# Kernel tuning notes

Hardware: AMD Instinct MI355X
Metric: run time of the kernel (lower is better)

Reference implementation:

```python
import jax, jax.numpy as jnp
import numpy as np

B, L, D, N, NBLK = 16, 2048, 256, 64, 6  # 6 S4D layers: blocks 1,2,3,5 + 2 inner layers of FS4Ddeq


def setup_inputs() -> dict:
    key = jax.random.key(0)
    ks = jax.random.split(key, 12)
    x = jax.random.normal(ks[0], (B, L), dtype=jnp.float32)
    W_emb = jax.random.normal(ks[1], (1, D), dtype=jnp.float32) * 0.1
    b_emb = jnp.zeros((D,), jnp.float32)
    # S4D parameters, stacked over the 6 layers
    log_dt = jax.random.uniform(ks[2], (NBLK, D), minval=float(np.log(1e-3)), maxval=float(np.log(1e-1)), dtype=jnp.float32)
    logAre = jnp.full((NBLK, D, N), float(np.log(0.5)), jnp.float32)
    Aim = jnp.broadcast_to(jnp.pi * jnp.arange(N, dtype=jnp.float32), (NBLK, D, N)) * jnp.ones((NBLK, D, N), jnp.float32)
    Cre = jax.random.normal(ks[3], (NBLK, D, N), dtype=jnp.float32) * (0.5 ** 0.5)
    Cim = jax.random.normal(ks[4], (NBLK, D, N), dtype=jnp.float32) * (0.5 ** 0.5)
    Dskip = jax.random.normal(ks[5], (NBLK, D), dtype=jnp.float32)
    Wout = jax.random.normal(ks[6], (NBLK, D, D), dtype=jnp.float32) / np.sqrt(D)
    bout = jnp.zeros((NBLK, D), jnp.float32)
    gamma = jnp.ones((NBLK, D), jnp.float32)
    beta = jnp.zeros((NBLK, D), jnp.float32)
    # feedforward of the FS4Ddeq block (feed_size=[B,L,emb_dim], feed_act='relu')
    feed_W1 = jax.random.normal(ks[7], (D, D), dtype=jnp.float32) / np.sqrt(D)
    feed_b1 = jnp.zeros((D,), jnp.float32)
    feed_W2 = jax.random.normal(ks[8], (D, D), dtype=jnp.float32) / np.sqrt(D)
    feed_b2 = jnp.zeros((D,), jnp.float32)
    fc_W = jax.random.normal(ks[9], (D, 2), dtype=jnp.float32) / np.sqrt(D)
    fc_b = jnp.zeros((2,), jnp.float32)
    return dict(x=x, W_emb=W_emb, b_emb=b_emb, log_dt=log_dt, logAre=logAre, Aim=Aim,
                Cre=Cre, Cim=Cim, Dskip=Dskip, Wout=Wout, bout=bout, gamma=gamma, beta=beta,
                feed_W1=feed_W1, feed_b1=feed_b1, feed_W2=feed_W2, feed_b2=feed_b2,
                fc_W=fc_W, fc_b=fc_b)


def _s4d_block(h, log_dt, logAre, Aim, Cre, Cim, Dskip, Wout, bout, gamma, beta):
    """Pre-norm (BN eval-mode) -> diagonal SSM (ZOH, FFT conv) -> GELU -> Linear -> residual."""
    _, Lh, _ = h.shape
    z = gamma * h + beta  # BatchNorm in eval mode with identity running stats
    dt = jnp.exp(log_dt)[:, None]                      # [D,1]
    A = -jnp.exp(logAre) + 1j * Aim                    # [D,N] diagonal state matrix
    dtA = dt * A                                       # [D,N]
    C = (Cre + 1j * Cim) * (jnp.exp(dtA) - 1.0) / A    # ZOH-discretized C*B
    # Vandermonde kernel K[d,l] = 2*Re sum_n C[d,n] * exp(dtA[d,n])^l
    vand = jnp.exp(dtA[:, :, None] * jnp.arange(Lh, dtype=jnp.float32))  # [D,N,L]
    K = 2.0 * jnp.einsum('dn,dnl->dl', C, vand).real   # [D,L]
    u = jnp.transpose(z, (0, 2, 1))                    # [B,D,L]
    kf = jnp.fft.rfft(K, n=2 * Lh)
    uf = jnp.fft.rfft(u, n=2 * Lh)
    y = jnp.fft.irfft(uf * kf, n=2 * Lh)[..., :Lh]     # causal conv
    y = y + Dskip[:, None] * u                         # feedthrough D
    y = jax.nn.gelu(jnp.transpose(y, (0, 2, 1)))       # [B,L,D]
    y = jnp.einsum('bld,de->ble', y, Wout) + bout      # output projection
    return y + h                                       # skip connection


def reference(x, W_emb, b_emb, log_dt, logAre, Aim, Cre, Cim, Dskip, Wout, bout,
              gamma, beta, feed_W1, feed_b1, feed_W2, feed_b2, fc_W, fc_b):
    h = x[..., None] @ W_emb + b_emb  # nn.Linear(1, emb_dim): [B,L,D]
    # layers 1,2,3,5: S4D blocks (dropout is identity in eval mode)
    for i in range(4):
        h = _s4d_block(h, log_dt[i], logAre[i], Aim[i], Cre[i], Cim[i],
                       Dskip[i], Wout[i], bout[i], gamma[i], beta[i])
    # layer4: FS4Ddeq_model with layers=2 inner S4D blocks + relu feed net + final relu + skip
    r = h
    for i in (4, 5):
        h = _s4d_block(h, log_dt[i], logAre[i], Aim[i], Cre[i], Cim[i],
                       Dskip[i], Wout[i], bout[i], gamma[i], beta[i])
    h = jax.nn.relu(h @ feed_W1 + feed_b1) @ feed_W2 + feed_b2
    h = jax.nn.relu(h + r)
    mean_y = jnp.mean(h, axis=1)       # [B,D]
    logits = mean_y @ fc_W + fc_b      # [B,2]
    return logits
```

## Files before the change

kernel.cpp:

```cpp
#include <hip/hip_runtime.h>
#include <hip/hip_fp16.h>
#include <math.h>

#define B_ 16
#define L_ 2048
#define D_ 256
#define N_ 64
#define NBLK_ 6
#define LC_ 128
#define NC_ 16

typedef _Float16 half8 __attribute__((ext_vector_type(8)));
typedef float f32x4 __attribute__((ext_vector_type(4)));

__device__ __forceinline__ unsigned short f2h(float f) {
  _Float16 h = (_Float16)f;
  return *(unsigned short*)&h;
}
__device__ __forceinline__ float h2f(unsigned short u) {
  _Float16 h = *(_Float16*)&u;
  return (float)h;
}

__global__ void precompute_kernel(const float* __restrict__ log_dt,
                                  const float* __restrict__ logAre,
                                  const float* __restrict__ Aim,
                                  const float* __restrict__ Cre,
                                  const float* __restrict__ Cim,
                                  float* __restrict__ wbuf,
                                  float* __restrict__ c2buf,
                                  float* __restrict__ wlbuf) {
  int idx = blockIdx.x * blockDim.x + threadIdx.x;
  if (idx >= NBLK_ * D_ * N_) return;
  int blk = idx >> 14;
  int rem = idx & 16383;
  int d = rem >> 6;
  int n = rem & 63;
  float dt   = expf(log_dt[blk * D_ + d]);
  float are  = -expf(logAre[idx]);
  float aim  = Aim[idx];
  float dtar = dt * are, dtai = dt * aim;
  float er = expf(dtar);
  float wr = er * cosf(dtai);
  float wi = er * sinf(dtai);
  float inv = 1.0f / (are * are + aim * aim);
  float wm1r = wr - 1.0f;
  float br = (wm1r * are + wi * aim) * inv;
  float bi = (wi * are - wm1r * aim) * inv;
  float crv = Cre[idx], civ = Cim[idx];
  float c2r = 2.0f * (crv * br - civ * bi);
  float c2i = 2.0f * (crv * bi + civ * br);
  float eL = expf((float)LC_ * dtar);
  float angL = (float)LC_ * dtai;
  float* wb = wbuf + (size_t)((blk << 8) + d) * 128;
  wb[n] = wr; wb[64 + n] = wi;
  float* cb = c2buf + (size_t)((blk << 8) + d) * 128;
  cb[n] = c2r; cb[64 + n] = c2i;
  wlbuf[2 * idx] = eL * cosf(angL); wlbuf[2 * idx + 1] = eL * sinf(angL);
}

__global__ __launch_bounds__(256) void embed_trans(const float* __restrict__ x,
    const float* __restrict__ wemb, const float* __restrict__ bemb,
    unsigned short* __restrict__ H, unsigned short* __restrict__ UT) {
  __shared__ __align__(16) unsigned short lds[64][136];
  int bi = blockIdx.x;
  int bc = bi >> 2, dq = bi & 3;
  int b = bc >> 4, ch = bc & 15;
  int tid = threadIdx.x;
  int tau0 = tid >> 4;
  int dl = (tid & 15) << 2;
  float w4[4], b4[4];
#pragma unroll
  for (int i = 0; i < 4; ++i) {
    w4[i] = wemb[dq * 64 + dl + i];
    b4[i] = bemb[dq * 64 + dl + i];
  }
  for (int tt = 0; tt < 128; tt += 16) {
    int l = ch * 128 + tt + tau0;
    float xv = x[b * L_ + l];
    ushort4 hv;
    float v0 = fmaf(xv, w4[0], b4[0]);
    float v1 = fmaf(xv, w4[1], b4[1]);
    float v2 = fmaf(xv, w4[2], b4[2]);
    float v3 = fmaf(xv, w4[3], b4[3]);
    hv.x = f2h(v0); hv.y = f2h(v1); hv.z = f2h(v2); hv.w = f2h(v3);
    lds[dl + 0][tt + tau0] = hv.x;
    lds[dl + 1][tt + tau0] = hv.y;
    lds[dl + 2][tt + tau0] = hv.z;
    lds[dl + 3][tt + tau0] = hv.w;
    *(ushort4*)(H + ((size_t)(b * L_ + l)) * D_ + dq * 64 + dl) = hv;
  }
  __syncthreads();
  int r = tid >> 2, seg = (tid & 3) << 5;
  unsigned short* dst = UT + ((size_t)((dq * 64 + r) * 256 + bc)) * 128 + seg;
  const unsigned short* srow = &lds[r][seg];
  *(uint4*)(dst + 0)  = *(const uint4*)(srow + 0);
  *(uint4*)(dst + 8)  = *(const uint4*)(srow + 8);
  *(uint4*)(dst + 16) = *(const uint4*)(srow + 16);
  *(uint4*)(dst + 24) = *(const uint4*)(srow + 24);
}

__global__ __launch_bounds__(512) void scan_fused(
    const unsigned short* __restrict__ UT,
    const float* __restrict__ WB, const float* __restrict__ C2B,
    const float* __restrict__ WLB,
    const float* __restrict__ gamma_, const float* __restrict__ beta_,
    const float* __restrict__ dskip,
    unsigned short* __restrict__ GT, int blk) {
  __shared__ __align__(16) unsigned short SLl[256 * 136];
  __shared__ __align__(16) unsigned short Bm1[128 * 136];
  __shared__ __align__(16) unsigned short Bm2[128 * 136];
  __shared__ float wc[256];
  __shared__ float Kt[128];
  __shared__ float Pb[128];
  __shared__ float Sb[128];
  int d = blockIdx.x;
  int tid = threadIdx.x, lane = tid & 63, w = tid >> 6;
  int wm = (w & 3) << 6;
  int wn = (w >> 2) << 6;
  int cn = lane & 15, rq = lane >> 4;
  int ko = rq << 3;
  const unsigned short* Au = UT + (size_t)d * 256 * 128;

  half8 afr[4][4];
#pragma unroll
  for (int kc2 = 0; kc2 < 4; ++kc2)
#pragma unroll
    for (int mf = 0; mf < 4; ++mf)
      afr[kc2][mf] = *(const half8*)(Au + (size_t)(wm + (mf << 4) + cn) * 128 + (kc2 << 5) + ko);

  if (tid < 128) wc[tid] = WB[(size_t)((blk << 8) + d) * 128 + tid];
  else if (tid < 256) wc[tid] = C2B[(size_t)((blk << 8) + d) * 128 + (tid - 128)];
  __syncthreads();
  int n = tid & 63;
  float gd = gamma_[blk * D_ + d], bd = beta_[blk * D_ + d], dsk = dskip[blk * D_ + d];
  {
    float wr = wc[n], wi = wc[64 + n];
    float c2r = wc[128 + n], c2i = wc[192 + n];
    int j0 = w << 4;
    float pr = 1.f, pi = 0.f, br = wr, bi = wi;
    int e = j0;
    while (e) {
      if (e & 1) { float tt = pr * br - pi * bi; pi = pr * bi + pi * br; pr = tt; }
      float t2 = br * br - bi * bi; bi = 2.f * br * bi; br = t2;
      e >>= 1;
    }
    for (int k2 = 0; k2 < 16; ++k2) {
      int j = j0 + k2;
      Bm1[n * 136 + (127 - j)]        = f2h(gd * pr);
      Bm1[(64 + n) * 136 + (127 - j)] = f2h(-gd * pi);
      float qr = pr * wr - pi * wi, qi = pr * wi + pi * wr;
      Bm2[j * 136 + n]      = f2h(c2r * qr - c2i * qi);
      Bm2[j * 136 + 64 + n] = f2h(c2r * qi + c2i * qr);
      float kc = c2r * pr - c2i * pi;
#pragma unroll
      for (int off = 1; off < 64; off <<= 1) kc += __shfl_xor(kc, off);
      if (n == 0) Kt[j] = kc + (j == 0 ? dsk : 0.f);
      pr = qr; pi = qi;
    }
  }
  if (tid < 64) {
    const float* wlp = WLB + (((size_t)((blk << 8) + d)) * 64 + tid) * 2;
    float wlr = wlp[0], wli = wlp[1];
    float nr = wlr - 1.f, ni = wli;
    float dr2 = wc[tid] - 1.f, di = wc[64 + tid];
    float iv = 1.f / (dr2 * dr2 + di * di);
    Sb[tid]      = bd * ((nr * dr2 + ni * di) * iv);
    Sb[64 + tid] = bd * (-((ni * dr2 - nr * di) * iv));
  }
  __syncthreads();

  {
    f32x4 acc[4][4];
#pragma unroll
    for (int a = 0; a < 4; ++a)
#pragma unroll
      for (int b2 = 0; b2 < 4; ++b2) acc[a][b2] = (f32x4){0.f, 0.f, 0.f, 0.f};
#pragma unroll
    for (int kc = 0; kc < 4; ++kc) {
      half8 bf4[4];
#pragma unroll
      for (int nf = 0; nf < 4; ++nf)
        bf4[nf] = *(const half8*)((const _Float16*)Bm1 + (wn + (nf << 4) + cn) * 136 + (kc << 5) + ko);
#pragma unroll
      for (int mf = 0; mf < 4; ++mf)
#pragma unroll
        for (int nf = 0; nf < 4; ++nf)
          acc[mf][nf] = __builtin_amdgcn_mfma_f32_16x16x32_f16(afr[kc][mf], bf4[nf], acc[mf][nf], 0, 0, 0);
    }
#pragma unroll
    for (int nf = 0; nf < 4; ++nf) {
      int nl = wn + (nf << 4) + cn;
      float sb = Sb[nl];
#pragma unroll
      for (int mf = 0; mf < 4; ++mf)
#pragma unroll
        for (int rr = 0; rr < 4; ++rr) {
          int row = wm + (mf << 4) + (rq << 2) + rr;
          SLl[row * 136 + nl] = f2h(acc[mf][nf][rr] + sb);
        }
    }
  }
  __syncthreads();

  if (tid < 128) {
    float ps = 0.f;
    for (int t2 = 0; t2 <= tid; ++t2) ps += Kt[t2];
    Pb[tid] = bd * ps;
  }
  for (int task = tid; task < 1024; task += 512) {
    int b = task >> 6, nn = task & 63;
    const float* wlp = WLB + (((size_t)((blk << 8) + d)) * 64 + nn) * 2;
    float wlr = wlp[0], wli = wlp[1];
    float Sr = 0.f, Sj = 0.f;
    int row0 = b << 4;
    float tr2 = h2f(SLl[row0 * 136 + nn]);
    float tj2 = h2f(SLl[row0 * 136 + 64 + nn]);
    for (int c = 0; c < NC_; ++c) {
      int row = row0 + c;
      float ntr = 0.f, ntj = 0.f;
      if (c < NC_ - 1) {
        ntr = h2f(SLl[(row + 1) * 136 + nn]);
        ntj = h2f(SLl[(row + 1) * 136 + 64 + nn]);
      }
      SLl[row * 136 + nn]      = f2h(Sr);
      SLl[row * 136 + 64 + nn] = f2h(Sj);
      float nSr = fmaf(wlr, Sr, fmaf(wli, Sj, tr2));
      Sj = fmaf(-wli, Sr, fmaf(wlr, Sj, tj2));
      Sr = nSr;
      tr2 = ntr; tj2 = ntj;
    }
  }
  __syncthreads();

  {
    int chunk = tid & 15, rg = tid >> 4;
#pragma unroll
    for (int it = 0; it < 4; ++it) {
      int trow = (it << 5) + rg;
      int tau0 = chunk << 3;
      unsigned short v[8];
#pragma unroll
      for (int i = 0; i < 8; ++i) {
        int tau = tau0 + i;
        v[i] = (tau <= trow) ? f2h(gd * Kt[trow - tau]) : (unsigned short)0;
      }
      *(uint4*)(Bm1 + (size_t)trow * 136 + tau0) = *(uint4*)v;
    }
  }
  __syncthreads();

  {
    f32x4 acc[4][4];
#pragma unroll
    for (int a = 0; a < 4; ++a)
#pragma unroll
      for (int b2 = 0; b2 < 4; ++b2) acc[a][b2] = (f32x4){0.f, 0.f, 0.f, 0.f};
#pragma unroll
    for (int kb = 0; kb < 8; ++kb) {
      int kc = (kb & 3) << 5;
      half8 af[4], bf4[4];
      if (kb < 4) {
#pragma unroll
        for (int mf = 0; mf < 4; ++mf) af[mf] = afr[kb][mf];
#pragma unroll
        for (int nf = 0; nf < 4; ++nf)
          bf4[nf] = *(const half8*)((const _Float16*)Bm1 + (wn + (nf << 4) + cn) * 136 + kc + ko);
      } else {
#pragma unroll
        for (int mf = 0; mf < 4; ++mf)
          af[mf] = *(const half8*)((const _Float16*)SLl + (wm + (mf << 4) + cn) * 136 + kc + ko);
#pragma unroll
        for (int nf = 0; nf < 4; ++nf)
          bf4[nf] = *(const half8*)((const _Float16*)Bm2 + (wn + (nf << 4) + cn) * 136 + kc + ko);
      }
#pragma unroll
      for (int mf = 0; mf < 4; ++mf)
#pragma unroll
        for (int nf = 0; nf < 4; ++nf)
          acc[mf][nf] = __builtin_amdgcn_mfma_f32_16x16x32_f16(af[mf], bf4[nf], acc[mf][nf], 0, 0, 0);
    }
    __syncthreads();
    unsigned short* epi = SLl;
#pragma unroll
    for (int nf = 0; nf < 4; ++nf) {
      int nl = wn + (nf << 4) + cn;
      float pb2 = Pb[nl];
#pragma unroll
      for (int mf = 0; mf < 4; ++mf)
#pragma unroll
        for (int rr = 0; rr < 4; ++rr) {
          int ml = wm + (mf << 4) + (rq << 2) + rr;
          float xx = acc[mf][nf][rr] + pb2;
          float x3 = xx * xx * xx;
          float inner = 0.7978845608028654f * fmaf(0.044715f, x3, xx);
          float e = __expf(-2.f * fabsf(inner));
          float th = (1.f - e) / (1.f + e);
          th = copysignf(th, inner);
          epi[ml * 136 + nl] = f2h(0.5f * xx * (1.f + th));
        }
    }
    __syncthreads();
    int mr = tid >> 1, hf = (tid & 1) << 6;
    size_t gb = ((size_t)d * 256 + mr) * 128 + hf;
#pragma unroll
    for (int k = 0; k < 8; ++k)
      *(uint4*)(GT + gb + k * 8) = *(const uint4*)&epi[mr * 136 + hf + k * 8];
  }
}

__global__ void wprep_kernel(const float* __restrict__ Wout, const float* __restrict__ fW1,
                             const float* __restrict__ fW2, unsigned short* __restrict__ WT) {
  __shared__ float tile[64][65];
  int wv = blockIdx.x >> 4;
  int tk = (blockIdx.x >> 2) & 3;
  int tn = blockIdx.x & 3;
  const float* src = (wv < 6) ? (Wout + (size_t)wv * 65536) : (wv == 6 ? fW1 : fW2);
  int r = threadIdx.x >> 4;
  int c = (threadIdx.x & 15) << 2;
  for (int rr = 0; rr < 64; rr += 16) {
    float4 v = *(const float4*)(src + (size_t)(tk * 64 + r + rr) * 256 + tn * 64 + c);
    tile[r + rr][c] = v.x; tile[r + rr][c + 1] = v.y;
    tile[r + rr][c + 2] = v.z; tile[r + rr][c + 3] = v.w;
  }
  __syncthreads();
  for (int rr = 0; rr < 64; rr += 16) {
    int n = r + rr;
    ushort4 o;
    o.x = f2h(tile[c + 0][n]); o.y = f2h(tile[c + 1][n]);
    o.z = f2h(tile[c + 2][n]); o.w = f2h(tile[c + 3][n]);
    *(ushort4*)(WT + (size_t)wv * 65536 + (size_t)(tn * 64 + n) * 256 + tk * 64 + c) = o;
  }
}

__global__ __launch_bounds__(256, 2) void gemm_gt(const unsigned short* __restrict__ GT,
    const unsigned short* __restrict__ Wt, const float* __restrict__ bias,
    const unsigned short* __restrict__ res, unsigned short* __restrict__ hout,
    unsigned short* __restrict__ ut_next) {
  __shared__ __align__(16) unsigned short smem[18432];
  unsigned short* As = smem;
  unsigned short* Bs = smem + 9216;
  int tid = threadIdx.x;
  int bid = blockIdx.x;
  int bc = bid & 255;
  int m0 = bc * 128, n0 = (bid >> 8) << 7;
  int lane = tid & 63, w = tid >> 6;
  int wm = (w & 1) << 6, wn = (w >> 1) << 6;
  int rb = tid >> 3, cb = (tid & 7) << 3;
  int dr = tid >> 2, sg = (tid & 3) << 5;
  f32x4 acc[4][4];
#pragma unroll
  for (int mf = 0; mf < 4; ++mf)
#pragma unroll
    for (int nf = 0; nf < 4; ++nf) acc[mf][nf] = (f32x4){0.f, 0.f, 0.f, 0.f};

  uint4 gv[4], bv[4];
  {
    const uint4* grow = (const uint4*)(GT + ((size_t)(dr * 256 + bc)) * 128 + sg);
    gv[0] = grow[0]; gv[1] = grow[1]; gv[2] = grow[2]; gv[3] = grow[3];
#pragma unroll
    for (int rr = 0; rr < 4; ++rr)
      bv[rr] = *(const uint4*)(Wt + (size_t)(n0 + rb + rr * 32) * 256 + cb);
  }
  for (int kb = 0; kb < 4; ++kb) {
    __syncthreads();
    const unsigned short* pv = (const unsigned short*)gv;
#pragma unroll
    for (int i = 0; i < 32; ++i) As[(sg + i) * 72 + dr] = pv[i];
#pragma unroll
    for (int rr = 0; rr < 4; ++rr) *(uint4*)&Bs[(rb + rr * 32) * 72 + cb] = bv[rr];
    __syncthreads();
    if (kb < 3) {
      int k0 = (kb + 1) << 6;
      const uint4* grow = (const uint4*)(GT + ((size_t)((k0 + dr) * 256 + bc)) * 128 + sg);
      gv[0] = grow[0]; gv[1] = grow[1]; gv[2] = grow[2]; gv[3] = grow[3];
#pragma unroll
      for (int rr = 0; rr < 4; ++rr)
        bv[rr] = *(const uint4*)(Wt + (size_t)(n0 + rb + rr * 32) * 256 + k0 + cb);
    }
#pragma unroll
    for (int kw = 0; kw < 2; ++kw) {
      int ko = (kw << 5) + ((lane >> 4) << 3);
      half8 af[4], bfr[4];
#pragma unroll
      for (int mf = 0; mf < 4; ++mf)
        af[mf] = *(const half8*)&As[(wm + (mf << 4) + (lane & 15)) * 72 + ko];
#pragma unroll
      for (int nf = 0; nf < 4; ++nf)
        bfr[nf] = *(const half8*)&Bs[(wn + (nf << 4) + (lane & 15)) * 72 + ko];
#pragma unroll
      for (int mf = 0; mf < 4; ++mf)
#pragma unroll
        for (int nf = 0; nf < 4; ++nf)
          acc[mf][nf] = __builtin_amdgcn_mfma_f32_16x16x32_f16(af[mf], bfr[nf], acc[mf][nf], 0, 0, 0);
    }
  }
  int cn = lane & 15, rq = lane >> 4;
  __syncthreads();
  unsigned short* epi = smem;
#pragma unroll
  for (int nf = 0; nf < 4; ++nf) {
    int nl = wn + (nf << 4) + cn;
    float bv2 = bias[n0 + nl];
#pragma unroll
    for (int mf = 0; mf < 4; ++mf)
#pragma unroll
      for (int r = 0; r < 4; ++r) {
        int ml = wm + (mf << 4) + (rq << 2) + r;
        float v = acc[mf][nf][r] + bv2 + h2f(res[(size_t)(m0 + ml) * 256 + n0 + nl]);
        epi[ml * 136 + nl] = f2h(v);
      }
  }
  __syncthreads();
  {
    int mr = tid >> 1, hf = (tid & 1) << 6;
    unsigned short* dst = hout + (size_t)(m0 + mr) * 256 + n0 + hf;
    const unsigned short* srow = epi + mr * 136 + hf;
#pragma unroll
    for (int k = 0; k < 8; ++k) *(uint4*)(dst + k * 8) = *(const uint4*)(srow + k * 8);
  }
  if (ut_next) {
    int nl = tid >> 1, h2 = (tid & 1) << 6;
    unsigned short* dst = ut_next + ((size_t)(n0 + nl) * 256 + bc) * 128 + h2;
#pragma unroll
    for (int k = 0; k < 8; ++k) {
      unsigned short v8[8];
#pragma unroll
      for (int e = 0; e < 8; ++e) v8[e] = epi[(h2 + k * 8 + e) * 136 + nl];
      *(uint4*)(dst + k * 8) = *(uint4*)v8;
    }
  }
}

__global__ __launch_bounds__(256, 2) void gemm_ffn(const unsigned short* __restrict__ A,
    const unsigned short* __restrict__ Wt, const float* __restrict__ bias,
    const unsigned short* __restrict__ res, unsigned short* __restrict__ outp) {
  __shared__ __align__(16) unsigned short smem[18432];
  unsigned short* As = smem;
  unsigned short* Bs = smem + 9216;
  int tid = threadIdx.x;
  int bid = blockIdx.x;
  int m0 = (bid & 255) << 7, n0 = (bid >> 8) << 7;
  int lane = tid & 63, w = tid >> 6;
  int wm = (w & 1) << 6, wn = (w >> 1) << 6;
  int r0 = tid >> 3;
  int c0 = (tid & 7) << 3;
  f32x4 acc[4][4];
#pragma unroll
  for (int mf = 0; mf < 4; ++mf)
#pragma unroll
    for (int nf = 0; nf < 4; ++nf) acc[mf][nf] = (f32x4){0.f, 0.f, 0.f, 0.f};

  uint4 av[4], bv[4];
#pragma unroll
  for (int rr = 0; rr < 4; ++rr) {
    int r = r0 + rr * 32;
    av[rr] = *(const uint4*)(A + (size_t)(m0 + r) * 256 + c0);
    bv[rr] = *(const uint4*)(Wt + (size_t)(n0 + r) * 256 + c0);
  }
  for (int kb = 0; kb < 4; ++kb) {
    __syncthreads();
#pragma unroll
    for (int rr = 0; rr < 4; ++rr) {
      int r = r0 + rr * 32;
      *(uint4*)&As[r * 72 + c0] = av[rr];
      *(uint4*)&Bs[r * 72 + c0] = bv[rr];
    }
    __syncthreads();
    if (kb < 3) {
      int k0 = (kb + 1) << 6;
#pragma unroll
      for (int rr = 0; rr < 4; ++rr) {
        int r = r0 + rr * 32;
        av[rr] = *(const uint4*)(A + (size_t)(m0 + r) * 256 + k0 + c0);
        bv[rr] = *(const uint4*)(Wt + (size_t)(n0 + r) * 256 + k0 + c0);
      }
    }
#pragma unroll
    for (int kw = 0; kw < 2; ++kw) {
      int ko = (kw << 5) + ((lane >> 4) << 3);
      half8 af[4], bfr[4];
#pragma unroll
      for (int mf = 0; mf < 4; ++mf)
        af[mf] = *(const half8*)&As[(wm + (mf << 4) + (lane & 15)) * 72 + ko];
#pragma unroll
      for (int nf = 0; nf < 4; ++nf)
        bfr[nf] = *(const half8*)&Bs[(wn + (nf << 4) + (lane & 15)) * 72 + ko];
#pragma unroll
      for (int mf = 0; mf < 4; ++mf)
#pragma unroll
        for (int nf = 0; nf < 4; ++nf)
          acc[mf][nf] = __builtin_amdgcn_mfma_f32_16x16x32_f16(af[mf], bfr[nf], acc[mf][nf], 0, 0, 0);
    }
  }
  int cn = lane & 15, rq = lane >> 4;
  __syncthreads();
  unsigned short* epi = smem;
#pragma unroll
  for (int nf = 0; nf < 4; ++nf) {
    int nl = wn + (nf << 4) + cn;
#pragma unroll
    for (int r = 0; r < 4; ++r) {
#pragma unroll
      for (int mf = 0; mf < 4; ++mf) {
        int ml = wm + (mf << 4) + (rq << 2) + r;
        epi[ml * 136 + nl] = f2h(acc[mf][nf][r]);
      }
    }
  }
  __syncthreads();
  int mr = tid >> 1, hf = (tid & 1) << 6;
  unsigned short* dst = outp + (size_t)(m0 + mr) * 256 + n0 + hf;
#pragma unroll
  for (int k = 0; k < 8; ++k) {
    uint4 c = *(const uint4*)&epi[mr * 136 + hf + k * 8];
    uint4 rv = (uint4){0, 0, 0, 0};
    if (res) rv = *(const uint4*)(res + (size_t)(m0 + mr) * 256 + n0 + hf + k * 8);
    const unsigned short* cp = (const unsigned short*)&c;
    const unsigned short* rp = (const unsigned short*)&rv;
    unsigned short o8[8];
#pragma unroll
    for (int e = 0; e < 8; ++e) {
      float v = h2f(cp[e]) + bias[n0 + hf + k * 8 + e];
      if (res) v += h2f(rp[e]);
      o8[e] = f2h(fmaxf(v, 0.f));
    }
    *(uint4*)(dst + k * 8) = *(uint4*)o8;
  }
}

__global__ void head1_kernel(const unsigned short* __restrict__ H, float* __restrict__ part) {
  int b = blockIdx.x, ls = blockIdx.y, d = threadIdx.x;
  const unsigned short* p = H + ((size_t)(b * L_ + ls * 128)) * D_ + d;
  float sum = 0.f;
  for (int l = 0; l < 128; ++l) sum += h2f(p[(size_t)l * D_]);
  part[(b * 16 + ls) * D_ + d] = sum;
}

__global__ void head2_kernel(const float* __restrict__ part, const float* __restrict__ fcW,
                             const float* __restrict__ fcb, float* __restrict__ out) {
  int b = blockIdx.x, d = threadIdx.x;
  float sum = 0.f;
  for (int i = 0; i < 16; ++i) sum += part[(b * 16 + i) * D_ + d];
  __shared__ float meanv[D_];
  meanv[d] = sum * (1.0f / (float)L_);
  __syncthreads();
  if (d < 2) {
    float accv = fcb[d];
    for (int k = 0; k < D_; ++k) accv = fmaf(meanv[k], fcW[k * 2 + d], accv);
    out[b * 2 + d] = accv;
  }
}

extern "C" void kernel_launch(void* const* d_in, const int* in_sizes, int n_in,
                              void* d_out, int out_size, void* d_ws, size_t ws_size,
                              hipStream_t stream) {
  const float* x      = (const float*)d_in[0];
  const float* W_emb  = (const float*)d_in[1];
  const float* b_emb  = (const float*)d_in[2];
  const float* log_dt = (const float*)d_in[3];
  const float* logAre = (const float*)d_in[4];
  const float* Aim    = (const float*)d_in[5];
  const float* Cre    = (const float*)d_in[6];
  const float* Cim    = (const float*)d_in[7];
  const float* Dskip  = (const float*)d_in[8];
  const float* Wout   = (const float*)d_in[9];
  const float* bout   = (const float*)d_in[10];
  const float* gamma_ = (const float*)d_in[11];
  const float* beta_  = (const float*)d_in[12];
  const float* fW1    = (const float*)d_in[13];
  const float* fb1    = (const float*)d_in[14];
  const float* fW2    = (const float*)d_in[15];
  const float* fb2    = (const float*)d_in[16];
  const float* fcW    = (const float*)d_in[17];
  const float* fcb    = (const float*)d_in[18];
  float* outp = (float*)d_out;

  const size_t HSZ = (size_t)B_ * L_ * D_;
  float* WB     = (float*)d_ws;
  float* C2B    = WB + (size_t)NBLK_ * D_ * 128;
  float* WLB    = C2B + (size_t)NBLK_ * D_ * 128;
  unsigned short* H   = (unsigned short*)(WLB + (size_t)NBLK_ * D_ * N_ * 2);
  unsigned short* R   = H + HSZ;
  unsigned short* UT  = R + HSZ;
  unsigned short* GT  = UT + HSZ;
  unsigned short* Gbf = GT;
  unsigned short* WT  = GT + HSZ;

  precompute_kernel<<<(NBLK_ * D_ * N_ + 255) / 256, 256, 0, stream>>>(
      log_dt, logAre, Aim, Cre, Cim, WB, C2B, WLB);
  wprep_kernel<<<128, 256, 0, stream>>>(Wout, fW1, fW2, WT);
  embed_trans<<<1024, 256, 0, stream>>>(x, W_emb, b_emb, H, UT);

  const unsigned short* hin_t[6]  = {H, H, H, H, R, H};
  unsigned short*       hout_t[6] = {H, H, H, R, H, H};
  for (int i = 0; i < 6; ++i) {
    scan_fused<<<256, 512, 0, stream>>>(UT, WB, C2B, WLB, gamma_, beta_, Dskip, GT, i);
    gemm_gt<<<512, 256, 0, stream>>>(
        GT, WT + (size_t)i * 65536, bout + i * D_, hin_t[i], hout_t[i],
        (i < 5) ? UT : nullptr);
  }
  gemm_ffn<<<512, 256, 0, stream>>>(H, WT + (size_t)6 * 65536, fb1, nullptr, Gbf);
  gemm_ffn<<<512, 256, 0, stream>>>(Gbf, WT + (size_t)7 * 65536, fb2, R, H);
  head1_kernel<<<dim3(16, 16), 256, 0, stream>>>(H, WB);
  head2_kernel<<<16, 256, 0, stream>>>(WB, fcW, fcb, outp);
}
```

Measured before the change: 542.9 us.

## Merge prep kernels, halve GEMM N-tile for more blocks, fuse head via atomic counter

Three setup kernels (parameter precompute, weight transpose, embedding) are merged into one launch that dispatches on block index. Both GEMM kernels drop from 128x128 to 128x64 tiles, doubling the grid to 1024 blocks, halving shared memory and raising launch bounds to 4 blocks per CU for better occupancy. The two head kernels become one, with a last-block-done atomic counter doing the final reduction. The aim is less launch overhead and better GPU fill, at the cost of more redundant A-tile loads across N-tiles.

```diff
diff --git a/kernel.cpp b/kernel.cpp
--- a/kernel.cpp
+++ b/kernel.cpp
@@ -22,82 +22,110 @@
   return (float)h;
 }
 
-__global__ void precompute_kernel(const float* __restrict__ log_dt,
-                                  const float* __restrict__ logAre,
-                                  const float* __restrict__ Aim,
-                                  const float* __restrict__ Cre,
-                                  const float* __restrict__ Cim,
-                                  float* __restrict__ wbuf,
-                                  float* __restrict__ c2buf,
-                                  float* __restrict__ wlbuf) {
-  int idx = blockIdx.x * blockDim.x + threadIdx.x;
-  if (idx >= NBLK_ * D_ * N_) return;
-  int blk = idx >> 14;
-  int rem = idx & 16383;
-  int d = rem >> 6;
-  int n = rem & 63;
-  float dt   = expf(log_dt[blk * D_ + d]);
-  float are  = -expf(logAre[idx]);
-  float aim  = Aim[idx];
-  float dtar = dt * are, dtai = dt * aim;
-  float er = expf(dtar);
-  float wr = er * cosf(dtai);
-  float wi = er * sinf(dtai);
-  float inv = 1.0f / (are * are + aim * aim);
-  float wm1r = wr - 1.0f;
-  float br = (wm1r * are + wi * aim) * inv;
-  float bi = (wi * are - wm1r * aim) * inv;
-  float crv = Cre[idx], civ = Cim[idx];
-  float c2r = 2.0f * (crv * br - civ * bi);
-  float c2i = 2.0f * (crv * bi + civ * br);
-  float eL = expf((float)LC_ * dtar);
-  float angL = (float)LC_ * dtai;
-  float* wb = wbuf + (size_t)((blk << 8) + d) * 128;
-  wb[n] = wr; wb[64 + n] = wi;
-  float* cb = c2buf + (size_t)((blk << 8) + d) * 128;
-  cb[n] = c2r; cb[64 + n] = c2i;
-  wlbuf[2 * idx] = eL * cosf(angL); wlbuf[2 * idx + 1] = eL * sinf(angL);
-}
-
-__global__ __launch_bounds__(256) void embed_trans(const float* __restrict__ x,
-    const float* __restrict__ wemb, const float* __restrict__ bemb,
-    unsigned short* __restrict__ H, unsigned short* __restrict__ UT) {
-  __shared__ __align__(16) unsigned short lds[64][136];
-  int bi = blockIdx.x;
-  int bc = bi >> 2, dq = bi & 3;
-  int b = bc >> 4, ch = bc & 15;
+__global__ __launch_bounds__(256) void prep_kernel(
+    const float* __restrict__ x, const float* __restrict__ wemb,
+    const float* __restrict__ bemb,
+    const float* __restrict__ log_dt, const float* __restrict__ logAre,
+    const float* __restrict__ Aim, const float* __restrict__ Cre,
+    const float* __restrict__ Cim,
+    const float* __restrict__ Wout, const float* __restrict__ fW1,
+    const float* __restrict__ fW2,
+    float* __restrict__ wbuf, float* __restrict__ c2buf,
+    float* __restrict__ wlbuf, unsigned short* __restrict__ WT,
+    unsigned short* __restrict__ H, unsigned short* __restrict__ UT,
+    int* __restrict__ cnt) {
+  __shared__ __align__(16) unsigned char ldsraw[17408];
+  int bid = blockIdx.x;
   int tid = threadIdx.x;
-  int tau0 = tid >> 4;
-  int dl = (tid & 15) << 2;
-  float w4[4], b4[4];
-#pragma unroll
-  for (int i = 0; i < 4; ++i) {
-    w4[i] = wemb[dq * 64 + dl + i];
-    b4[i] = bemb[dq * 64 + dl + i];
-  }
-  for (int tt = 0; tt < 128; tt += 16) {
-    int l = ch * 128 + tt + tau0;
-    float xv = x[b * L_ + l];
-    ushort4 hv;
-    float v0 = fmaf(xv, w4[0], b4[0]);
-    float v1 = fmaf(xv, w4[1], b4[1]);
-    float v2 = fmaf(xv, w4[2], b4[2]);
-    float v3 = fmaf(xv, w4[3], b4[3]);
-    hv.x = f2h(v0); hv.y = f2h(v1); hv.z = f2h(v2); hv.w = f2h(v3);
-    lds[dl + 0][tt + tau0] = hv.x;
-    lds[dl + 1][tt + tau0] = hv.y;
-    lds[dl + 2][tt + tau0] = hv.z;
-    lds[dl + 3][tt + tau0] = hv.w;
-    *(ushort4*)(H + ((size_t)(b * L_ + l)) * D_ + dq * 64 + dl) = hv;
-  }
-  __syncthreads();
-  int r = tid >> 2, seg = (tid & 3) << 5;
-  unsigned short* dst = UT + ((size_t)((dq * 64 + r) * 256 + bc)) * 128 + seg;
-  const unsigned short* srow = &lds[r][seg];
-  *(uint4*)(dst + 0)  = *(const uint4*)(srow + 0);
-  *(uint4*)(dst + 8)  = *(const uint4*)(srow + 8);
-  *(uint4*)(dst + 16) = *(const uint4*)(srow + 16);
-  *(uint4*)(dst + 24) = *(const uint4*)(srow + 24);
+  if (bid < 384) {
+    if (bid == 0 && tid < 16) cnt[tid] = 0;
+    int idx = bid * 256 + tid;
+    if (idx < NBLK_ * D_ * N_) {
+      int blk = idx >> 14;
+      int rem = idx & 16383;
+      int d = rem >> 6;
+      int n = rem & 63;
+      float dt   = expf(log_dt[blk * D_ + d]);
+      float are  = -expf(logAre[idx]);
+      float aim  = Aim[idx];
+      float dtar = dt * are, dtai = dt * aim;
+      float er = expf(dtar);
+      float wr = er * cosf(dtai);
+      float wi = er * sinf(dtai);
+      float inv = 1.0f / (are * are + aim * aim);
+      float wm1r = wr - 1.0f;
+      float br = (wm1r * are + wi * aim) * inv;
+      float bi2 = (wi * are - wm1r * aim) * inv;
+      float crv = Cre[idx], civ = Cim[idx];
+      float c2r = 2.0f * (crv * br - civ * bi2);
+      float c2i = 2.0f * (crv * bi2 + civ * br);
+      float eL = expf((float)LC_ * dtar);
+      float angL = (float)LC_ * dtai;
+      float* wb = wbuf + (size_t)((blk << 8) + d) * 128;
+      wb[n] = wr; wb[64 + n] = wi;
+      float* cb = c2buf + (size_t)((blk << 8) + d) * 128;
+      cb[n] = c2r; cb[64 + n] = c2i;
+      wlbuf[2 * idx] = eL * cosf(angL); wlbuf[2 * idx + 1] = eL * sinf(angL);
+    }
+  } else if (bid < 512) {
+    float (*tile)[65] = (float (*)[65])ldsraw;
+    int b2 = bid - 384;
+    int wv = b2 >> 4;
+    int tk = (b2 >> 2) & 3;
+    int tn = b2 & 3;
+    const float* src = (wv < 6) ? (Wout + (size_t)wv * 65536) : (wv == 6 ? fW1 : fW2);
+    int r = tid >> 4;
+    int c = (tid & 15) << 2;
+    for (int rr = 0; rr < 64; rr += 16) {
+      float4 v = *(const float4*)(src + (size_t)(tk * 64 + r + rr) * 256 + tn * 64 + c);
+      tile[r + rr][c] = v.x; tile[r + rr][c + 1] = v.y;
+      tile[r + rr][c + 2] = v.z; tile[r + rr][c + 3] = v.w;
+    }
+    __syncthreads();
+    for (int rr = 0; rr < 64; rr += 16) {
+      int n = r + rr;
+      ushort4 o;
+      o.x = f2h(tile[c + 0][n]); o.y = f2h(tile[c + 1][n]);
+      o.z = f2h(tile[c + 2][n]); o.w = f2h(tile[c + 3][n]);
+      *(ushort4*)(WT + (size_t)wv * 65536 + (size_t)(tn * 64 + n) * 256 + tk * 64 + c) = o;
+    }
+  } else {
+    unsigned short (*lds)[136] = (unsigned short (*)[136])ldsraw;
+    int bi = bid - 512;
+    int bc = bi >> 2, dq = bi & 3;
+    int b = bc >> 4, ch = bc & 15;
+    int tau0 = tid >> 4;
+    int dl = (tid & 15) << 2;
+    float w4[4], b4[4];
+#pragma unroll
+    for (int i = 0; i < 4; ++i) {
+      w4[i] = wemb[dq * 64 + dl + i];
+      b4[i] = bemb[dq * 64 + dl + i];
+    }
+    for (int tt = 0; tt < 128; tt += 16) {
+      int l = ch * 128 + tt + tau0;
+      float xv = x[b * L_ + l];
+      ushort4 hv;
+      float v0 = fmaf(xv, w4[0], b4[0]);
+      float v1 = fmaf(xv, w4[1], b4[1]);
+      float v2 = fmaf(xv, w4[2], b4[2]);
+      float v3 = fmaf(xv, w4[3], b4[3]);
+      hv.x = f2h(v0); hv.y = f2h(v1); hv.z = f2h(v2); hv.w = f2h(v3);
+      lds[dl + 0][tt + tau0] = hv.x;
+      lds[dl + 1][tt + tau0] = hv.y;
+      lds[dl + 2][tt + tau0] = hv.z;
+      lds[dl + 3][tt + tau0] = hv.w;
+      *(ushort4*)(H + ((size_t)(b * L_ + l)) * D_ + dq * 64 + dl) = hv;
+    }
+    __syncthreads();
+    int r = tid >> 2, seg = (tid & 3) << 5;
+    unsigned short* dst = UT + ((size_t)((dq * 64 + r) * 256 + bc)) * 128 + seg;
+    const unsigned short* srow = &lds[r][seg];
+    *(uint4*)(dst + 0)  = *(const uint4*)(srow + 0);
+    *(uint4*)(dst + 8)  = *(const uint4*)(srow + 8);
+    *(uint4*)(dst + 16) = *(const uint4*)(srow + 16);
+    *(uint4*)(dst + 24) = *(const uint4*)(srow + 24);
+  }
 }
 
 __global__ __launch_bounds__(512) void scan_fused(
@@ -309,57 +337,33 @@
   }
 }
 
-__global__ void wprep_kernel(const float* __restrict__ Wout, const float* __restrict__ fW1,
-                             const float* __restrict__ fW2, unsigned short* __restrict__ WT) {
-  __shared__ float tile[64][65];
-  int wv = blockIdx.x >> 4;
-  int tk = (blockIdx.x >> 2) & 3;
-  int tn = blockIdx.x & 3;
-  const float* src = (wv < 6) ? (Wout + (size_t)wv * 65536) : (wv == 6 ? fW1 : fW2);
-  int r = threadIdx.x >> 4;
-  int c = (threadIdx.x & 15) << 2;
-  for (int rr = 0; rr < 64; rr += 16) {
-    float4 v = *(const float4*)(src + (size_t)(tk * 64 + r + rr) * 256 + tn * 64 + c);
-    tile[r + rr][c] = v.x; tile[r + rr][c + 1] = v.y;
-    tile[r + rr][c + 2] = v.z; tile[r + rr][c + 3] = v.w;
-  }
-  __syncthreads();
-  for (int rr = 0; rr < 64; rr += 16) {
-    int n = r + rr;
-    ushort4 o;
-    o.x = f2h(tile[c + 0][n]); o.y = f2h(tile[c + 1][n]);
-    o.z = f2h(tile[c + 2][n]); o.w = f2h(tile[c + 3][n]);
-    *(ushort4*)(WT + (size_t)wv * 65536 + (size_t)(tn * 64 + n) * 256 + tk * 64 + c) = o;
-  }
-}
-
-__global__ __launch_bounds__(256, 2) void gemm_gt(const unsigned short* __restrict__ GT,
+__global__ __launch_bounds__(256, 4) void gemm_gt(const unsigned short* __restrict__ GT,
     const unsigned short* __restrict__ Wt, const float* __restrict__ bias,
     const unsigned short* __restrict__ res, unsigned short* __restrict__ hout,
     unsigned short* __restrict__ ut_next) {
-  __shared__ __align__(16) unsigned short smem[18432];
+  __shared__ __align__(16) unsigned short smem[9216 + 4608];
   unsigned short* As = smem;
   unsigned short* Bs = smem + 9216;
   int tid = threadIdx.x;
   int bid = blockIdx.x;
   int bc = bid & 255;
-  int m0 = bc * 128, n0 = (bid >> 8) << 7;
+  int m0 = bc << 7, n0 = (bid >> 8) << 6;
   int lane = tid & 63, w = tid >> 6;
-  int wm = (w & 1) << 6, wn = (w >> 1) << 6;
+  int wm = (w & 1) << 6, wn = (w >> 1) << 5;
   int rb = tid >> 3, cb = (tid & 7) << 3;
   int dr = tid >> 2, sg = (tid & 3) << 5;
-  f32x4 acc[4][4];
+  f32x4 acc[4][2];
 #pragma unroll
   for (int mf = 0; mf < 4; ++mf)
 #pragma unroll
-    for (int nf = 0; nf < 4; ++nf) acc[mf][nf] = (f32x4){0.f, 0.f, 0.f, 0.f};
-
-  uint4 gv[4], bv[4];
+    for (int nf = 0; nf < 2; ++nf) acc[mf][nf] = (f32x4){0.f, 0.f, 0.f, 0.f};
+
+  uint4 gv[4], bv[2];
   {
     const uint4* grow = (const uint4*)(GT + ((size_t)(dr * 256 + bc)) * 128 + sg);
     gv[0] = grow[0]; gv[1] = grow[1]; gv[2] = grow[2]; gv[3] = grow[3];
 #pragma unroll
-    for (int rr = 0; rr < 4; ++rr)
+    for (int rr = 0; rr < 2; ++rr)
       bv[rr] = *(const uint4*)(Wt + (size_t)(n0 + rb + rr * 32) * 256 + cb);
   }
   for (int kb = 0; kb < 4; ++kb) {
@@ -368,30 +372,30 @@
 #pragma unroll
     for (int i = 0; i < 32; ++i) As[(sg + i) * 72 + dr] = pv[i];
 #pragma unroll
-    for (int rr = 0; rr < 4; ++rr) *(uint4*)&Bs[(rb + rr * 32) * 72 + cb] = bv[rr];
+    for (int rr = 0; rr < 2; ++rr) *(uint4*)&Bs[(rb + rr * 32) * 72 + cb] = bv[rr];
     __syncthreads();
     if (kb < 3) {
       int k0 = (kb + 1) << 6;
       const uint4* grow = (const uint4*)(GT + ((size_t)((k0 + dr) * 256 + bc)) * 128 + sg);
       gv[0] = grow[0]; gv[1] = grow[1]; gv[2] = grow[2]; gv[3] = grow[3];
 #pragma unroll
-      for (int rr = 0; rr < 4; ++rr)
+      for (int rr = 0; rr < 2; ++rr)
         bv[rr] = *(const uint4*)(Wt + (size_t)(n0 + rb + rr * 32) * 256 + k0 + cb);
     }
 #pragma unroll
     for (int kw = 0; kw < 2; ++kw) {
       int ko = (kw << 5) + ((lane >> 4) << 3);
-      half8 af[4], bfr[4];
+      half8 af[4], bfr[2];
 #pragma unroll
       for (int mf = 0; mf < 4; ++mf)
         af[mf] = *(const half8*)&As[(wm + (mf << 4) + (lane & 15)) * 72 + ko];
 #pragma unroll
-      for (int nf = 0; nf < 4; ++nf)
+      for (int nf = 0; nf < 2; ++nf)
         bfr[nf] = *(const half8*)&Bs[(wn + (nf << 4) + (lane & 15)) * 72 + ko];
 #pragma unroll
       for (int mf = 0; mf < 4; ++mf)
 #pragma unroll
-        for (int nf = 0; nf < 4; ++nf)
+        for (int nf = 0; nf < 2; ++nf)
           acc[mf][nf] = __builtin_amdgcn_mfma_f32_16x16x32_f16(af[mf], bfr[nf], acc[mf][nf], 0, 0, 0);
     }
   }
@@ -399,7 +403,7 @@
   __syncthreads();
   unsigned short* epi = smem;
 #pragma unroll
-  for (int nf = 0; nf < 4; ++nf) {
+  for (int nf = 0; nf < 2; ++nf) {
     int nl = wn + (nf << 4) + cn;
     float bv2 = bias[n0 + nl];
 #pragma unroll
@@ -408,88 +412,86 @@
       for (int r = 0; r < 4; ++r) {
         int ml = wm + (mf << 4) + (rq << 2) + r;
         float v = acc[mf][nf][r] + bv2 + h2f(res[(size_t)(m0 + ml) * 256 + n0 + nl]);
-        epi[ml * 136 + nl] = f2h(v);
+        epi[ml * 72 + nl] = f2h(v);
       }
   }
   __syncthreads();
   {
-    int mr = tid >> 1, hf = (tid & 1) << 6;
+    int mr = tid >> 1, hf = (tid & 1) << 5;
     unsigned short* dst = hout + (size_t)(m0 + mr) * 256 + n0 + hf;
-    const unsigned short* srow = epi + mr * 136 + hf;
-#pragma unroll
-    for (int k = 0; k < 8; ++k) *(uint4*)(dst + k * 8) = *(const uint4*)(srow + k * 8);
+    const unsigned short* srow = epi + mr * 72 + hf;
+#pragma unroll
+    for (int k = 0; k < 4; ++k) *(uint4*)(dst + k * 8) = *(const uint4*)(srow + k * 8);
   }
   if (ut_next) {
-    int nl = tid >> 1, h2 = (tid & 1) << 6;
-    unsigned short* dst = ut_next + ((size_t)(n0 + nl) * 256 + bc) * 128 + h2;
-#pragma unroll
-    for (int k = 0; k < 8; ++k) {
+    int nl = tid >> 2, sg2 = (tid & 3) << 5;
+    unsigned short* dst = ut_next + ((size_t)(n0 + nl) * 256 + bc) * 128 + sg2;
+#pragma unroll
+    for (int k = 0; k < 4; ++k) {
       unsigned short v8[8];
 #pragma unroll
-      for (int e = 0; e < 8; ++e) v8[e] = epi[(h2 + k * 8 + e) * 136 + nl];
+      for (int e = 0; e < 8; ++e) v8[e] = epi[(sg2 + k * 8 + e) * 72 + nl];
       *(uint4*)(dst + k * 8) = *(uint4*)v8;
     }
   }
 }
 
-__global__ __launch_bounds__(256, 2) void gemm_ffn(const unsigned short* __restrict__ A,
+__global__ __launch_bounds__(256, 4) void gemm_ffn(const unsigned short* __restrict__ A,
     const unsigned short* __restrict__ Wt, const float* __restrict__ bias,
     const unsigned short* __restrict__ res, unsigned short* __restrict__ outp) {
-  __shared__ __align__(16) unsigned short smem[18432];
+  __shared__ __align__(16) unsigned short smem[9216 + 4608];
   unsigned short* As = smem;
   unsigned short* Bs = smem + 9216;
   int tid = threadIdx.x;
   int bid = blockIdx.x;
-  int m0 = (bid & 255) << 7, n0 = (bid >> 8) << 7;
+  int m0 = (bid & 255) << 7, n0 = (bid >> 8) << 6;
   int lane = tid & 63, w = tid >> 6;
-  int wm = (w & 1) << 6, wn = (w >> 1) << 6;
+  int wm = (w & 1) << 6, wn = (w >> 1) << 5;
   int r0 = tid >> 3;
   int c0 = (tid & 7) << 3;
-  f32x4 acc[4][4];
+  f32x4 acc[4][2];
 #pragma unroll
   for (int mf = 0; mf < 4; ++mf)
 #pragma unroll
-    for (int nf = 0; nf < 4; ++nf) acc[mf][nf] = (f32x4){0.f, 0.f, 0.f, 0.f};
-
-  uint4 av[4], bv[4];
-#pragma unroll
-  for (int rr = 0; rr < 4; ++rr) {
-    int r = r0 + rr * 32;
-    av[rr] = *(const uint4*)(A + (size_t)(m0 + r) * 256 + c0);
-    bv[rr] = *(const uint4*)(Wt + (size_t)(n0 + r) * 256 + c0);
-  }
+    for (int nf = 0; nf < 2; ++nf) acc[mf][nf] = (f32x4){0.f, 0.f, 0.f, 0.f};
+
+  uint4 av[4], bv[2];
+#pragma unroll
+  for (int rr = 0; rr < 4; ++rr)
+    av[rr] = *(const uint4*)(A + (size_t)(m0 + r0 + rr * 32) * 256 + c0);
+#pragma unroll
+  for (int rr = 0; rr < 2; ++rr)
+    bv[rr] = *(const uint4*)(Wt + (size_t)(n0 + r0 + rr * 32) * 256 + c0);
   for (int kb = 0; kb < 4; ++kb) {
     __syncthreads();
 #pragma unroll
-    for (int rr = 0; rr < 4; ++rr) {
-      int r = r0 + rr * 32;
-      *(uint4*)&As[r * 72 + c0] = av[rr];
-      *(uint4*)&Bs[r * 72 + c0] = bv[rr];
-    }
+    for (int rr = 0; rr < 4; ++rr) *(uint4*)&As[(r0 + rr * 32) * 72 + c0] = av[rr];
+#pragma unroll
+    for (int rr = 0; rr < 2; ++rr) *(uint4*)&Bs[(r0 + rr * 32) * 72 + c0] = bv[rr];
     __syncthreads();
     if (kb < 3) {
       int k0 = (kb + 1) << 6;
 #pragma unroll
-      for (int rr = 0; rr < 4; ++rr) {
-        int r = r0 + rr * 32;
-        av[rr] = *(const uint4*)(A + (size_t)(m0 + r) * 256 + k0 + c0);
-        bv[rr] = *(const uint4*)(Wt + (size_t)(n0 + r) * 256 + k0 + c0);
-      }
+      for (int rr = 0; rr < 4; ++rr)
+        av[rr] = *(const uint4*)(A + (size_t)(m0 + r0 + rr * 32) * 256 + k0 + c0);
+#pragma unroll
+      for (int rr = 0; rr < 2; ++rr)
+        bv[rr] = *(const uint4*)(Wt + (size_t)(n0 + r0 + rr * 32) * 256 + k0 + c0);
     }
 #pragma unroll
     for (int kw = 0; kw < 2; ++kw) {
       int ko = (kw << 5) + ((lane >> 4) << 3);
-      half8 af[4], bfr[4];
+      half8 af[4], bfr[2];
 #pragma unroll
       for (int mf = 0; mf < 4; ++mf)
         af[mf] = *(const half8*)&As[(wm + (mf << 4) + (lane & 15)) * 72 + ko];
 #pragma unroll
-      for (int nf = 0; nf < 4; ++nf)
+      for (int nf = 0; nf < 2; ++nf)
         bfr[nf] = *(const half8*)&Bs[(wn + (nf << 4) + (lane & 15)) * 72 + ko];
 #pragma unroll
       for (int mf = 0; mf < 4; ++mf)
 #pragma unroll
-        for (int nf = 0; nf < 4; ++nf)
+        for (int nf = 0; nf < 2; ++nf)
           acc[mf][nf] = __builtin_amdgcn_mfma_f32_16x16x32_f16(af[mf], bfr[nf], acc[mf][nf], 0, 0, 0);
     }
   }
@@ -497,23 +499,23 @@
   __syncthreads();
   unsigned short* epi = smem;
 #pragma unroll
-  for (int nf = 0; nf < 4; ++nf) {
+  for (int nf = 0; nf < 2; ++nf) {
     int nl = wn + (nf << 4) + cn;
 #pragma unroll
     for (int r = 0; r < 4; ++r) {
 #pragma unroll
       for (int mf = 0; mf < 4; ++mf) {
         int ml = wm + (mf << 4) + (rq << 2) + r;
-        epi[ml * 136 + nl] = f2h(acc[mf][nf][r]);
+        epi[ml * 72 + nl] = f2h(acc[mf][nf][r]);
       }
     }
   }
   __syncthreads();
-  int mr = tid >> 1, hf = (tid & 1) << 6;
+  int mr = tid >> 1, hf = (tid & 1) << 5;
   unsigned short* dst = outp + (size_t)(m0 + mr) * 256 + n0 + hf;
 #pragma unroll
-  for (int k = 0; k < 8; ++k) {
-    uint4 c = *(const uint4*)&epi[mr * 136 + hf + k * 8];
+  for (int k = 0; k < 4; ++k) {
+    uint4 c = *(const uint4*)&epi[mr * 72 + hf + k * 8];
     uint4 rv = (uint4){0, 0, 0, 0};
     if (res) rv = *(const uint4*)(res + (size_t)(m0 + mr) * 256 + n0 + hf + k * 8);
     const unsigned short* cp = (const unsigned short*)&c;
@@ -529,26 +531,35 @@
   }
 }
 
-__global__ void head1_kernel(const unsigned short* __restrict__ H, float* __restrict__ part) {
+__global__ __launch_bounds__(256) void head_kernel(const unsigned short* __restrict__ H,
+    float* __restrict__ part, int* __restrict__ cnt,
+    const float* __restrict__ fcW, const float* __restrict__ fcb,
+    float* __restrict__ out) {
+  __shared__ float meanv[D_];
+  __shared__ int lastFlag;
   int b = blockIdx.x, ls = blockIdx.y, d = threadIdx.x;
   const unsigned short* p = H + ((size_t)(b * L_ + ls * 128)) * D_ + d;
   float sum = 0.f;
   for (int l = 0; l < 128; ++l) sum += h2f(p[(size_t)l * D_]);
   part[(b * 16 + ls) * D_ + d] = sum;
-}
-
-__global__ void head2_kernel(const float* __restrict__ part, const float* __restrict__ fcW,
-                             const float* __restrict__ fcb, float* __restrict__ out) {
-  int b = blockIdx.x, d = threadIdx.x;
-  float sum = 0.f;
-  for (int i = 0; i < 16; ++i) sum += part[(b * 16 + i) * D_ + d];
-  __shared__ float meanv[D_];
-  meanv[d] = sum * (1.0f / (float)L_);
-  __syncthreads();
-  if (d < 2) {
-    float accv = fcb[d];
-    for (int k = 0; k < D_; ++k) accv = fmaf(meanv[k], fcW[k * 2 + d], accv);
-    out[b * 2 + d] = accv;
+  __syncthreads();
+  if (d == 0) {
+    __threadfence();
+    lastFlag = (atomicAdd(&cnt[b], 1) == 15) ? 1 : 0;
+  }
+  __syncthreads();
+  if (lastFlag) {
+    __threadfence();
+    const volatile float* vp = part;
+    float s = 0.f;
+    for (int i = 0; i < 16; ++i) s += vp[(b * 16 + i) * D_ + d];
+    meanv[d] = s * (1.0f / (float)L_);
+    __syncthreads();
+    if (d < 2) {
+      float accv = fcb[d];
+      for (int k = 0; k < D_; ++k) accv = fmaf(meanv[k], fcW[k * 2 + d], accv);
+      out[b * 2 + d] = accv;
+    }
   }
 }
 
@@ -586,22 +597,20 @@
   unsigned short* GT  = UT + HSZ;
   unsigned short* Gbf = GT;
   unsigned short* WT  = GT + HSZ;
-
-  precompute_kernel<<<(NBLK_ * D_ * N_ + 255) / 256, 256, 0, stream>>>(
-      log_dt, logAre, Aim, Cre, Cim, WB, C2B, WLB);
-  wprep_kernel<<<128, 256, 0, stream>>>(Wout, fW1, fW2, WT);
-  embed_trans<<<1024, 256, 0, stream>>>(x, W_emb, b_emb, H, UT);
+  int* cnt = (int*)(WT + (size_t)8 * 65536);
+
+  prep_kernel<<<1536, 256, 0, stream>>>(x, W_emb, b_emb, log_dt, logAre, Aim, Cre, Cim,
+                                        Wout, fW1, fW2, WB, C2B, WLB, WT, H, UT, cnt);
 
   const unsigned short* hin_t[6]  = {H, H, H, H, R, H};
   unsigned short*       hout_t[6] = {H, H, H, R, H, H};
   for (int i = 0; i < 6; ++i) {
     scan_fused<<<256, 512, 0, stream>>>(UT, WB, C2B, WLB, gamma_, beta_, Dskip, GT, i);
-    gemm_gt<<<512, 256, 0, stream>>>(
+    gemm_gt<<<1024, 256, 0, stream>>>(
         GT, WT + (size_t)i * 65536, bout + i * D_, hin_t[i], hout_t[i],
         (i < 5) ? UT : nullptr);
   }
-  gemm_ffn<<<512, 256, 0, stream>>>(H, WT + (size_t)6 * 65536, fb1, nullptr, Gbf);
-  gemm_ffn<<<512, 256, 0, stream>>>(Gbf, WT + (size_t)7 * 65536, fb2, R, H);
-  head1_kernel<<<dim3(16, 16), 256, 0, stream>>>(H, WB);
-  head2_kernel<<<16, 256, 0, stream>>>(WB, fcW, fcb, outp);
-}
+  gemm_ffn<<<1024, 256, 0, stream>>>(H, WT + (size_t)6 * 65536, fb1, nullptr, Gbf);
+  gemm_ffn<<<1024, 256, 0, stream>>>(Gbf, WT + (size_t)7 * 65536, fb2, R, H);
+  head_kernel<<<dim3(16, 16), 256, 0, stream>>>(H, WB, cnt, fcW, fcb, outp);
+}
```

After: 538.6 us. About the same (-0.8%).
